# Kernel optimization log

Hardware: AMD Instinct MI355X
Metric: run time of the kernel (lower is better)

## Reference

```python
import jax, jax.numpy as jnp
import numpy as np

B, N, IN_DIM, SLOT_DIM, NUM_SLOTS, NUM_ITERS = 64, 4096, 256, 256, 8, 3
LN_EPS = 1e-5


def _ln(x, g, b):
    m = jnp.mean(x, axis=-1, keepdims=True)
    v = jnp.mean(jnp.square(x - m), axis=-1, keepdims=True)
    return (x - m) * jax.lax.rsqrt(v + LN_EPS) * g + b


def setup_inputs() -> dict:
    key = jax.random.key(0)
    ks = jax.random.split(key, 16)
    D, I = SLOT_DIM, IN_DIM
    s = 0.02
    return {
        "inputs": jax.random.normal(ks[0], (B, N, I), jnp.float32),
        "slots_noise": jax.random.normal(ks[1], (B, NUM_SLOTS, D), jnp.float32),
        "slots_mu": jax.random.normal(ks[2], (1, 1, D), jnp.float32),
        "slots_log_sigma": jnp.zeros((1, 1, D), jnp.float32),
        "ln_in_g": jnp.ones((I,), jnp.float32), "ln_in_b": jnp.zeros((I,), jnp.float32),
        "ln_s_g": jnp.ones((D,), jnp.float32), "ln_s_b": jnp.zeros((D,), jnp.float32),
        "ln_m_g": jnp.ones((D,), jnp.float32), "ln_m_b": jnp.zeros((D,), jnp.float32),
        "Wq": jax.random.normal(ks[3], (D, D), jnp.float32) * s,
        "Wk": jax.random.normal(ks[4], (I, D), jnp.float32) * s,
        "Wv": jax.random.normal(ks[5], (I, D), jnp.float32) * s,
        "gru_w_ih": jax.random.normal(ks[6], (3 * D, D), jnp.float32) * s,
        "gru_w_hh": jax.random.normal(ks[7], (3 * D, D), jnp.float32) * s,
        "gru_b_ih": jnp.zeros((3 * D,), jnp.float32),
        "gru_b_hh": jnp.zeros((3 * D,), jnp.float32),
        "mlp_w1": jax.random.normal(ks[8], (D, 4 * D), jnp.float32) * s,
        "mlp_b1": jnp.zeros((4 * D,), jnp.float32),
        "mlp_w2": jax.random.normal(ks[9], (4 * D, D), jnp.float32) * s,
        "mlp_b2": jnp.zeros((D,), jnp.float32),
    }


def reference(inputs, slots_noise, slots_mu, slots_log_sigma, ln_in_g, ln_in_b,
              ln_s_g, ln_s_b, ln_m_g, ln_m_b, Wq, Wk, Wv,
              gru_w_ih, gru_w_hh, gru_b_ih, gru_b_hh,
              mlp_w1, mlp_b1, mlp_w2, mlp_b2):
    D = SLOT_DIM
    # slot init: mu + sigma * noise
    slots = slots_mu + jnp.exp(slots_log_sigma) * slots_noise  # [B, S, D]
    x = _ln(inputs, ln_in_g, ln_in_b)                          # [B, N, I]
    k = x @ Wk                                                 # [B, N, D]
    v = x @ Wv                                                 # [B, N, D]
    scale = 1.0 / jnp.sqrt(jnp.float32(D))
    attn = None
    for _ in range(NUM_ITERS):
        slots_prev = slots
        s_n = _ln(slots, ln_s_g, ln_s_b)
        q = s_n @ Wq                                           # [B, S, D]
        logits = jnp.einsum('bnd,bmd->bnm', k, q) * scale      # [B, N, S]
        attn = jax.nn.softmax(logits, axis=-1)                 # softmax over slots
        attn_nrm = attn / (jnp.sum(attn, axis=1, keepdims=True) + 1e-8)
        updates = jnp.einsum('bnm,bnd->bmd', attn_nrm, v)      # [B, S, D]
        # GRUCell (PyTorch semantics)
        gi = updates @ gru_w_ih.T + gru_b_ih                   # [B, S, 3D]
        gh = slots_prev @ gru_w_hh.T + gru_b_hh
        gi_r, gi_z, gi_n = jnp.split(gi, 3, axis=-1)
        gh_r, gh_z, gh_n = jnp.split(gh, 3, axis=-1)
        r = jax.nn.sigmoid(gi_r + gh_r)
        z = jax.nn.sigmoid(gi_z + gh_z)
        n = jnp.tanh(gi_n + r * gh_n)
        slots = (1.0 - z) * n + z * slots_prev
        # residual MLP
        h = jax.nn.relu(_ln(slots, ln_m_g, ln_m_b) @ mlp_w1 + mlp_b1)
        slots = slots + h @ mlp_w2 + mlp_b2
    return slots, jnp.transpose(attn, (0, 2, 1))
```

## Files before the change

### kernel.cpp

```cpp
#include <hip/hip_runtime.h>


typedef unsigned short u16;
typedef __attribute__((ext_vector_type(8))) short bf16x8;
typedef __attribute__((ext_vector_type(4))) float f32x4;

#define MFMA16(a, b, c) __builtin_amdgcn_mfma_f32_16x16x32_bf16((a), (b), (c), 0, 0, 0)

__device__ __forceinline__ u16 f2bf(float f) {
  union { float f; unsigned u; } v; v.f = f;
  unsigned r = (v.u + 0x7fffu + ((v.u >> 16) & 1u)) >> 16;
  return (u16)r;
}
__device__ __forceinline__ float sigm(float x) { return 1.f / (1.f + __expf(-x)); }
__device__ __forceinline__ float tanh_f(float x) { return 1.f - 2.f / (1.f + __expf(2.f * x)); }

__global__ __launch_bounds__(256) void prep_kernel(
    const float* __restrict__ Wq, const float* __restrict__ Wk, const float* __restrict__ Wv,
    const float* __restrict__ wih, const float* __restrict__ whh,
    const float* __restrict__ w1, const float* __restrict__ w2,
    u16* __restrict__ wkB, u16* __restrict__ wqT, u16* __restrict__ wvT,
    u16* __restrict__ wihB, u16* __restrict__ whhB, u16* __restrict__ w1T, u16* __restrict__ w2T) {
  const int bid = blockIdx.x;
  const int tid = threadIdx.x;
  if (bid < 160) {
    __shared__ float tile[64][65];
    const float* src; u16* dst; int R, C, t;
    if (bid < 16)      { src = Wq; dst = wqT; R = 256;  C = 256;  t = bid; }
    else if (bid < 32) { src = Wv; dst = wvT; R = 256;  C = 256;  t = bid - 16; }
    else if (bid < 96) { src = w1; dst = w1T; R = 1024; C = 256;  t = bid - 32; }
    else               { src = w2; dst = w2T; R = 256;  C = 1024; t = bid - 96; }
    const int tilesJ = C >> 6;
    const int i0 = (t / tilesJ) * 64, j0 = (t % tilesJ) * 64;
    const int c = tid & 63, r0 = tid >> 6;
#pragma unroll
    for (int rr = 0; rr < 16; rr++) {
      int row = rr * 4 + r0;
      tile[row][c] = src[(size_t)(j0 + row) * R + i0 + c];
    }
    __syncthreads();
#pragma unroll
    for (int rr = 0; rr < 16; rr++) {
      int row = rr * 4 + r0;
      dst[(size_t)(i0 + row) * C + j0 + c] = f2bf(tile[c][row]);
    }
  } else {
    int gid = (bid - 160) * 256 + tid;
    for (int i4 = gid; i4 < 114688; i4 += 64 * 256) {
      int i = i4 * 4;
      const float* s; u16* d; int off;
      if (i < 65536) { s = Wk; d = wkB; off = i; }
      else if (i < 262144) { s = wih; d = wihB; off = i - 65536; }
      else { s = whh; d = whhB; off = i - 262144; }
      float4 v = *reinterpret_cast<const float4*>(s + off);
      unsigned lo = (unsigned)f2bf(v.x) | ((unsigned)f2bf(v.y) << 16);
      unsigned hi = (unsigned)f2bf(v.z) | ((unsigned)f2bf(v.w) << 16);
      *reinterpret_cast<uint2*>(d + off) = make_uint2(lo, hi);
    }
  }
}

__device__ __forceinline__ void ln_row16(const float (*src)[264], u16 (*dst)[264],
                                         const float* __restrict__ g, const float* __restrict__ bb,
                                         int wave, int lane) {
  int row = wave;
  if (row < 8) {
    float4 v = *reinterpret_cast<const float4*>(&src[row][lane * 4]);
    float s = v.x + v.y + v.z + v.w;
    float sq = v.x * v.x + v.y * v.y + v.z * v.z + v.w * v.w;
#pragma unroll
    for (int m = 1; m < 64; m <<= 1) { s += __shfl_xor(s, m); sq += __shfl_xor(sq, m); }
    float mu = s * (1.f / 256.f);
    float var = sq * (1.f / 256.f) - mu * mu;
    float rstd = rsqrtf(fmaxf(var, 0.f) + 1e-5f);
    float4 gg = *reinterpret_cast<const float4*>(&g[lane * 4]);
    float4 bv = *reinterpret_cast<const float4*>(&bb[lane * 4]);
    unsigned lo = (unsigned)f2bf((v.x - mu) * rstd * gg.x + bv.x) |
                  ((unsigned)f2bf((v.y - mu) * rstd * gg.y + bv.y) << 16);
    unsigned hi = (unsigned)f2bf((v.z - mu) * rstd * gg.z + bv.z) |
                  ((unsigned)f2bf((v.w - mu) * rstd * gg.w + bv.w) << 16);
    *reinterpret_cast<uint2*>(&dst[row][lane * 4]) = make_uint2(lo, hi);
  } else if (row < 16) {
    *reinterpret_cast<uint2*>(&dst[row][lane * 4]) = make_uint2(0, 0);
  }
}

__global__ __launch_bounds__(1024, 4) void slot_kernel(
    float* __restrict__ slots, u16* __restrict__ qg, float* __restrict__ cd,
    const float* __restrict__ wsY, const float* __restrict__ wsS,
    const u16* __restrict__ wvT, const u16* __restrict__ wihB, const u16* __restrict__ whhB,
    const u16* __restrict__ w1T, const u16* __restrict__ w2T, const u16* __restrict__ wqT,
    const u16* __restrict__ wkB,
    const float* __restrict__ bih, const float* __restrict__ bhh,
    const float* __restrict__ b1v, const float* __restrict__ b2v,
    const float* __restrict__ g_in, const float* __restrict__ b_in,
    const float* __restrict__ g_s, const float* __restrict__ b_s,
    const float* __restrict__ g_m, const float* __restrict__ b_m,
    const float* __restrict__ s_mu, const float* __restrict__ s_ls,
    const float* __restrict__ noise,
    float* __restrict__ d_out, int do_update) {
  __shared__ alignas(16) char pool[58368];
  u16 (*h_lds)[1032] = reinterpret_cast<u16(*)[1032]>(pool);
  u16 (*u_lds)[264] = reinterpret_cast<u16(*)[264]>(pool);
  u16 (*uv_lds)[264] = reinterpret_cast<u16(*)[264]>(pool + 8448);
  u16 (*sb_lds)[264] = reinterpret_cast<u16(*)[264]>(pool + 16896);
  u16 (*m_lds)[264] = reinterpret_cast<u16(*)[264]>(pool + 33024);
  float (*ns_lds)[264] = reinterpret_cast<float(*)[264]>(pool + 41472);
  u16 (*q_lds)[264] = reinterpret_cast<u16(*)[264]>(pool + 41472);
  __shared__ float sS0[16], sS1[16], sInv[16];
  __shared__ float redq[16][4][4][2];

  const int b = blockIdx.x;
  const int tid = threadIdx.x;
  const int lane = tid & 63, wave = tid >> 6;
  const int quad = lane >> 4, col = lane & 15;
  const int i256 = tid & 255, s4 = tid >> 8;
  const f32x4 vzero = {0.f, 0.f, 0.f, 0.f};

  if (do_update) {
    if (tid < 16) {
      float S0 = 0.f, S1 = 0.f;
      if (tid < 8) {
        for (int c = 0; c < 8; c++) {
          S0 += wsS[((b * 8 + c) * 8 + tid) * 2 + 0];
          S1 += wsS[((b * 8 + c) * 8 + tid) * 2 + 1];
        }
      }
      sS0[tid] = S0; sS1[tid] = S1; sInv[tid] = 1.f / (S0 + 1e-8f);
    }
#pragma unroll
    for (int r = 0; r < 4; r++) {
      int s = s4 + r * 4;
      sb_lds[s][i256] = (s < 8) ? f2bf(slots[(size_t)(b * 8 + s) * 256 + i256]) : (u16)0;
    }
    __syncthreads();
    {
      float gv = g_in[i256], bv = b_in[i256];
#pragma unroll
      for (int r = 0; r < 4; r++) {
        int s = s4 + r * 4;
        if (s < 8) {
          float y = 0.f;
#pragma unroll
          for (int c = 0; c < 8; c++) y += wsY[((size_t)((b * 8 + c) * 8 + s)) * 256 + i256];
          u_lds[s][i256] = f2bf((gv * (y - sS1[s]) + bv * sS0[s]) * sInv[s]);
        } else {
          u_lds[s][i256] = 0;
        }
      }
    }
    __syncthreads();
    {
      bf16x8 af[8];
#pragma unroll
      for (int k = 0; k < 8; k++)
        af[k] = *reinterpret_cast<const bf16x8*>(&u_lds[col][k * 32 + quad * 8]);
      int ct = wave;
      f32x4 acc = vzero;
#pragma unroll
      for (int k = 0; k < 8; k++) {
        bf16x8 bf = *reinterpret_cast<const bf16x8*>(wvT + (size_t)(ct * 16 + col) * 256 + k * 32 + quad * 8);
        acc = MFMA16(af[k], bf, acc);
      }
#pragma unroll
      for (int r = 0; r < 4; r++) {
        int s = quad * 4 + r;
        uv_lds[s][ct * 16 + col] = (s < 8) ? f2bf(acc[r]) : (u16)0;
      }
    }
    __syncthreads();
    {
      bf16x8 afu[8], afs[8];
#pragma unroll
      for (int k = 0; k < 8; k++) {
        afu[k] = *reinterpret_cast<const bf16x8*>(&uv_lds[col][k * 32 + quad * 8]);
        afs[k] = *reinterpret_cast<const bf16x8*>(&sb_lds[col][k * 32 + quad * 8]);
      }
      int d = wave * 16 + col;
      f32x4 a_ir = vzero, a_iz = vzero, a_in = vzero, a_hr = vzero, a_hz = vzero, a_hn = vzero;
#pragma unroll
      for (int k = 0; k < 8; k++) {
        int ko = k * 32 + quad * 8;
        a_ir = MFMA16(afu[k], *reinterpret_cast<const bf16x8*>(wihB + (size_t)(d)*256 + ko), a_ir);
        a_iz = MFMA16(afu[k], *reinterpret_cast<const bf16x8*>(wihB + (size_t)(256 + d) * 256 + ko), a_iz);
        a_in = MFMA16(afu[k], *reinterpret_cast<const bf16x8*>(wihB + (size_t)(512 + d) * 256 + ko), a_in);
        a_hr = MFMA16(afs[k], *reinterpret_cast<const bf16x8*>(whhB + (size_t)(d)*256 + ko), a_hr);
        a_hz = MFMA16(afs[k], *reinterpret_cast<const bf16x8*>(whhB + (size_t)(256 + d) * 256 + ko), a_hz);
        a_hn = MFMA16(afs[k], *reinterpret_cast<const bf16x8*>(whhB + (size_t)(512 + d) * 256 + ko), a_hn);
      }
      float bihr = bih[d], bihz = bih[256 + d], bihn = bih[512 + d];
      float bhhr = bhh[d], bhhz = bhh[256 + d], bhhn = bhh[512 + d];
#pragma unroll
      for (int r = 0; r < 4; r++) {
        int s = quad * 4 + r;
        float rg = sigm(a_ir[r] + bihr + a_hr[r] + bhhr);
        float zg = sigm(a_iz[r] + bihz + a_hz[r] + bhhz);
        float ng = tanh_f(a_in[r] + bihn + rg * (a_hn[r] + bhhn));
        float prev = (s < 8) ? slots[(size_t)(b * 8 + s) * 256 + d] : 0.f;
        float ns = (1.f - zg) * ng + zg * prev;
        ns_lds[s][d] = (s < 8) ? ns : 0.f;
      }
    }
    __syncthreads();
    ln_row16(ns_lds, m_lds, g_m, b_m, wave, lane);
    __syncthreads();
    {
      bf16x8 af[8];
#pragma unroll
      for (int k = 0; k < 8; k++)
        af[k] = *reinterpret_cast<const bf16x8*>(&m_lds[col][k * 32 + quad * 8]);
      for (int cc = 0; cc < 4; cc++) {
        int ct = wave * 4 + cc;
        f32x4 acc = vzero;
#pragma unroll
        for (int k = 0; k < 8; k++) {
          bf16x8 bf = *reinterpret_cast<const bf16x8*>(w1T + (size_t)(ct * 16 + col) * 256 + k * 32 + quad * 8);
          acc = MFMA16(af[k], bf, acc);
        }
        float bb = b1v[ct * 16 + col];
#pragma unroll
        for (int r = 0; r < 4; r++) {
          int s = quad * 4 + r;
          float h = fmaxf(acc[r] + bb, 0.f);
          h_lds[s][ct * 16 + col] = (s < 8) ? f2bf(h) : (u16)0;
        }
      }
    }
    __syncthreads();
    {
      int ct = wave;
      f32x4 acc = vzero;
      for (int k = 0; k < 32; k++) {
        bf16x8 af = *reinterpret_cast<const bf16x8*>(&h_lds[col][k * 32 + quad * 8]);
        bf16x8 bf = *reinterpret_cast<const bf16x8*>(w2T + (size_t)(ct * 16 + col) * 1024 + k * 32 + quad * 8);
        acc = MFMA16(af, bf, acc);
      }
      int d = ct * 16 + col;
      float bb = b2v[d];
#pragma unroll
      for (int r = 0; r < 4; r++) {
        int s = quad * 4 + r;
        if (s < 8) {
          float fin = ns_lds[s][d] + acc[r] + bb;
          slots[(size_t)(b * 8 + s) * 256 + d] = fin;
          d_out[(size_t)(b * 8 + s) * 256 + d] = fin;
          ns_lds[s][d] = fin;
        }
      }
    }
    __syncthreads();
  } else {
#pragma unroll
    for (int r = 0; r < 4; r++) {
      int s = s4 + r * 4;
      float v = 0.f;
      if (s < 8) {
        v = s_mu[i256] + __expf(s_ls[i256]) * noise[(size_t)(b * 8 + s) * 256 + i256];
        slots[(size_t)(b * 8 + s) * 256 + i256] = v;
      }
      ns_lds[s][i256] = v;
    }
    __syncthreads();
  }

  ln_row16(ns_lds, m_lds, g_s, b_s, wave, lane);
  __syncthreads();
  {
    bf16x8 af[8];
#pragma unroll
    for (int k = 0; k < 8; k++)
      af[k] = *reinterpret_cast<const bf16x8*>(&m_lds[col][k * 32 + quad * 8]);
    int ct = wave;
    f32x4 acc = vzero;
#pragma unroll
    for (int k = 0; k < 8; k++) {
      bf16x8 bf = *reinterpret_cast<const bf16x8*>(wqT + (size_t)(ct * 16 + col) * 256 + k * 32 + quad * 8);
      acc = MFMA16(af[k], bf, acc);
    }
#pragma unroll
    for (int r = 0; r < 4; r++) {
      int s = quad * 4 + r;
      q_lds[s][ct * 16 + col] = (s < 8) ? f2bf(acc[r]) : (u16)0;
    }
  }
  __syncthreads();
  {
    bf16x8 af[8];
#pragma unroll
    for (int k = 0; k < 8; k++)
      af[k] = *reinterpret_cast<const bf16x8*>(&q_lds[col][k * 32 + quad * 8]);
    float cacc[4] = {0.f, 0.f, 0.f, 0.f}, dacc[4] = {0.f, 0.f, 0.f, 0.f};
    int ct = wave;
    f32x4 acc = vzero;
#pragma unroll
    for (int k = 0; k < 8; k++) {
      bf16x8 bf = *reinterpret_cast<const bf16x8*>(wkB + (size_t)(ct * 16 + col) * 256 + k * 32 + quad * 8);
      acc = MFMA16(af[k], bf, acc);
    }
    int i = ct * 16 + col;
    float gi_ = g_in[i] * 0.0625f, bi_ = b_in[i] * 0.0625f;
#pragma unroll
    for (int r = 0; r < 4; r++) {
      int s = quad * 4 + r;
      float qkv = acc[r];
      float qgv = (s < 8) ? gi_ * qkv : 0.f;
      qg[(size_t)(b * 16 + s) * 256 + i] = f2bf(qgv);
      cacc[r] -= qgv;
      dacc[r] += (s < 8) ? bi_ * qkv : 0.f;
    }
#pragma unroll
    for (int r = 0; r < 4; r++) {
#pragma unroll
      for (int m = 1; m < 16; m <<= 1) {
        cacc[r] += __shfl_xor(cacc[r], m);
        dacc[r] += __shfl_xor(dacc[r], m);
      }
    }
    if (col == 0) {
#pragma unroll
      for (int r = 0; r < 4; r++) {
        redq[wave][quad][r][0] = cacc[r];
        redq[wave][quad][r][1] = dacc[r];
      }
    }
    __syncthreads();
    if (tid < 16) {
      int qd = tid >> 2, r = tid & 3;
      float c = 0.f, dd = 0.f;
      for (int w = 0; w < 16; w++) { c += redq[w][qd][r][0]; dd += redq[w][qd][r][1]; }
      cd[(b * 16 + tid) * 2 + 0] = c;
      cd[(b * 16 + tid) * 2 + 1] = dd;
    }
  }
}

template <int PASS>
__global__ __launch_bounds__(512, 4) void attn_kernel(
    const float* __restrict__ x, u16* __restrict__ xb, float2* __restrict__ stats2,
    const u16* __restrict__ qg, const float* __restrict__ cd,
    float* __restrict__ out, float* __restrict__ wsY, float* __restrict__ wsS) {
  __shared__ alignas(16) u16 x_lds[64][264];
  __shared__ alignas(16) u16 a2t[16][72];
  __shared__ float2 stats_lds[64];
  __shared__ float2 red2[4][8];

  const int chunk = blockIdx.x, b = blockIdx.y;
  const int tid = threadIdx.x;
  const int lane = tid & 63, wave = tid >> 6;
  const int quad = lane >> 4, col = lane & 15;

  for (int idx = tid; idx < 288; idx += 512)
    reinterpret_cast<unsigned*>(&a2t[8][0])[idx] = 0;

  bf16x8 bfrag[8];
#pragma unroll
  for (int k = 0; k < 8; k++)
    bfrag[k] = *reinterpret_cast<const bf16x8*>(qg + (size_t)(b * 16 + col) * 256 + k * 32 + quad * 8);
  const float2 cdv = *reinterpret_cast<const float2*>(cd + (b * 16 + col) * 2);

  f32x4 Yacc[2];
  Yacc[0] = {0.f, 0.f, 0.f, 0.f};
  Yacc[1] = {0.f, 0.f, 0.f, 0.f};
  float s0a = 0.f, s1a = 0.f;
  float* out_attn = out + 131072;

  float4 pf0[8];
  uint2 pf1[8];
  float2 pfs;
  {
    const int nb0 = chunk * 512;
    if (PASS == 0) {
#pragma unroll
      for (int p = 0; p < 8; p++)
        pf0[p] = *reinterpret_cast<const float4*>(x + (size_t)(b * 4096 + nb0 + wave * 8 + p) * 256 + lane * 4);
    } else {
#pragma unroll
      for (int p = 0; p < 8; p++)
        pf1[p] = *reinterpret_cast<const uint2*>(xb + (size_t)(b * 4096 + nb0 + wave * 8 + p) * 256 + lane * 4);
      if (tid < 64) pfs = stats2[(size_t)b * 4096 + nb0 + tid];
    }
  }

  for (int g = 0; g < 8; g++) {
    const int nb = chunk * 512 + g * 64;
    __syncthreads();
    if (PASS == 0) {
#pragma unroll
      for (int p = 0; p < 8; p++) {
        int row = wave * 8 + p;
        float4 v = pf0[p];
        float s = v.x + v.y + v.z + v.w;
        float sq = v.x * v.x + v.y * v.y + v.z * v.z + v.w * v.w;
#pragma unroll
        for (int m = 1; m < 64; m <<= 1) { s += __shfl_xor(s, m); sq += __shfl_xor(sq, m); }
        float mu = s * (1.f / 256.f);
        float var = sq * (1.f / 256.f) - mu * mu;
        float rstd = rsqrtf(fmaxf(var, 0.f) + 1e-5f);
        float2 st = make_float2(rstd, rstd * mu);
        if (lane == 0) {
          stats_lds[row] = st;
          stats2[(size_t)b * 4096 + nb + row] = st;
        }
        unsigned lo = (unsigned)f2bf(v.x) | ((unsigned)f2bf(v.y) << 16);
        unsigned hi = (unsigned)f2bf(v.z) | ((unsigned)f2bf(v.w) << 16);
        *reinterpret_cast<uint2*>(&x_lds[row][lane * 4]) = make_uint2(lo, hi);
        *reinterpret_cast<uint2*>(xb + (size_t)(b * 4096 + nb + row) * 256 + lane * 4) = make_uint2(lo, hi);
      }
    } else {
#pragma unroll
      for (int p = 0; p < 8; p++) {
        int row = wave * 8 + p;
        *reinterpret_cast<uint2*>(&x_lds[row][lane * 4]) = pf1[p];
      }
      if (tid < 64) stats_lds[tid] = pfs;
    }
    __syncthreads();
    if (g < 7) {
      const int nbn = nb + 64;
      if (PASS == 0) {
#pragma unroll
        for (int p = 0; p < 8; p++)
          pf0[p] = *reinterpret_cast<const float4*>(x + (size_t)(b * 4096 + nbn + wave * 8 + p) * 256 + lane * 4);
      } else {
#pragma unroll
        for (int p = 0; p < 8; p++)
          pf1[p] = *reinterpret_cast<const uint2*>(xb + (size_t)(b * 4096 + nbn + wave * 8 + p) * 256 + lane * 4);
        if (tid < 64) pfs = stats2[(size_t)b * 4096 + nbn + tid];
      }
    }
    if (wave < 4) {
      const int rowbase = wave * 16;
      f32x4 acc = {0.f, 0.f, 0.f, 0.f};
#pragma unroll
      for (int k = 0; k < 8; k++) {
        bf16x8 af = *reinterpret_cast<const bf16x8*>(&x_lds[rowbase + col][k * 32 + quad * 8]);
        acc = MFMA16(af, bfrag[k], acc);
      }
      float at[4], rmx[4], rmy[4];
#pragma unroll
      for (int r = 0; r < 4; r++) {
        float2 rm = stats_lds[rowbase + quad * 4 + r];
        rmx[r] = rm.x; rmy[r] = rm.y;
        float lg = rm.x * acc[r] + rm.y * cdv.x + cdv.y;
        float mx = lg;
        mx = fmaxf(mx, __shfl_xor(mx, 1));
        mx = fmaxf(mx, __shfl_xor(mx, 2));
        mx = fmaxf(mx, __shfl_xor(mx, 4));
        float e = __expf(lg - mx);
        float sm = e;
        sm += __shfl_xor(sm, 1); sm += __shfl_xor(sm, 2); sm += __shfl_xor(sm, 4);
        at[r] = e / sm;
      }
      if (col < 8) {
#pragma unroll
        for (int r = 0; r < 4; r++) {
          int n_loc = rowbase + quad * 4 + r;
          out_attn[(size_t)(b * 8 + col) * 4096 + nb + n_loc] = at[r];
          a2t[col][n_loc] = f2bf(at[r] * rmx[r]);
          s0a += at[r];
          s1a += at[r] * rmy[r];
        }
      }
    }
    __syncthreads();
    {
      bf16x8 af0 = *reinterpret_cast<const bf16x8*>(&a2t[col][quad * 8]);
      bf16x8 af1 = *reinterpret_cast<const bf16x8*>(&a2t[col][32 + quad * 8]);
#pragma unroll
      for (int cc = 0; cc < 2; cc++) {
        int ib = (wave * 2 + cc) * 16 + col;
        union { short s[8]; bf16x8 v; } b0, b1;
#pragma unroll
        for (int j = 0; j < 8; j++) {
          b0.s[j] = (short)x_lds[quad * 8 + j][ib];
          b1.s[j] = (short)x_lds[32 + quad * 8 + j][ib];
        }
        Yacc[cc] = MFMA16(af0, b0.v, Yacc[cc]);
        Yacc[cc] = MFMA16(af1, b1.v, Yacc[cc]);
      }
    }
  }
  if (quad < 2) {
#pragma unroll
    for (int cc = 0; cc < 2; cc++) {
      int i = (wave * 2 + cc) * 16 + col;
#pragma unroll
      for (int r = 0; r < 4; r++) {
        int s = quad * 4 + r;
        wsY[(size_t)((b * 8 + chunk) * 8 + s) * 256 + i] = Yacc[cc][r];
      }
    }
  }
  s0a += __shfl_xor(s0a, 16); s0a += __shfl_xor(s0a, 32);
  s1a += __shfl_xor(s1a, 16); s1a += __shfl_xor(s1a, 32);
  if (wave < 4 && lane < 8) red2[wave][lane] = make_float2(s0a, s1a);
  __syncthreads();
  if (tid < 8) {
    float S0 = 0.f, S1 = 0.f;
#pragma unroll
    for (int w = 0; w < 4; w++) { S0 += red2[w][tid].x; S1 += red2[w][tid].y; }
    wsS[((b * 8 + chunk) * 8 + tid) * 2 + 0] = S0;
    wsS[((b * 8 + chunk) * 8 + tid) * 2 + 1] = S1;
  }
}

extern "C" void kernel_launch(void* const* d_in, const int* in_sizes, int n_in,
                              void* d_out, int out_size, void* d_ws, size_t ws_size,
                              hipStream_t stream) {
  const float* inputs = (const float*)d_in[0];
  const float* noise = (const float*)d_in[1];
  const float* s_mu = (const float*)d_in[2];
  const float* s_ls = (const float*)d_in[3];
  const float* g_in = (const float*)d_in[4];
  const float* b_in = (const float*)d_in[5];
  const float* g_s = (const float*)d_in[6];
  const float* b_s = (const float*)d_in[7];
  const float* g_m = (const float*)d_in[8];
  const float* b_m = (const float*)d_in[9];
  const float* Wq = (const float*)d_in[10];
  const float* Wk = (const float*)d_in[11];
  const float* Wv = (const float*)d_in[12];
  const float* wih = (const float*)d_in[13];
  const float* whh = (const float*)d_in[14];
  const float* bih = (const float*)d_in[15];
  const float* bhh = (const float*)d_in[16];
  const float* w1 = (const float*)d_in[17];
  const float* b1v = (const float*)d_in[18];
  const float* w2 = (const float*)d_in[19];
  const float* b2v = (const float*)d_in[20];
  float* out = (float*)d_out;

  size_t o = 0;
  auto take = [&](size_t bytes) {
    void* p = (char*)d_ws + o;
    o += (bytes + 255) & ~(size_t)255;
    return p;
  };
  float* slots = (float*)take((size_t)64 * 8 * 256 * 4);
  u16* qg = (u16*)take((size_t)64 * 16 * 256 * 2);
  float* cd = (float*)take((size_t)64 * 16 * 2 * 4);
  float* wsY = (float*)take((size_t)64 * 8 * 8 * 256 * 4);
  float* wsS = (float*)take((size_t)64 * 8 * 8 * 2 * 4);
  u16* wkB = (u16*)take((size_t)65536 * 2);
  u16* wqT = (u16*)take((size_t)65536 * 2);
  u16* wvT = (u16*)take((size_t)65536 * 2);
  u16* wihB = (u16*)take((size_t)196608 * 2);
  u16* whhB = (u16*)take((size_t)196608 * 2);
  u16* w1T = (u16*)take((size_t)262144 * 2);
  u16* w2T = (u16*)take((size_t)262144 * 2);
  u16* xb = (u16*)take((size_t)64 * 4096 * 256 * 2);
  float2* stats2 = (float2*)take((size_t)64 * 4096 * 8);

  prep_kernel<<<224, 256, 0, stream>>>(Wq, Wk, Wv, wih, whh, w1, w2,
                                       wkB, wqT, wvT, wihB, whhB, w1T, w2T);
  slot_kernel<<<64, 1024, 0, stream>>>(slots, qg, cd, wsY, wsS,
                                       wvT, wihB, whhB, w1T, w2T, wqT, wkB,
                                       bih, bhh, b1v, b2v,
                                       g_in, b_in, g_s, b_s, g_m, b_m,
                                       s_mu, s_ls, noise, out, 0);
  for (int it = 0; it < 3; it++) {
    if (it == 0)
      attn_kernel<0><<<dim3(8, 64), 512, 0, stream>>>(inputs, xb, stats2, qg, cd, out, wsY, wsS);
    else
      attn_kernel<1><<<dim3(8, 64), 512, 0, stream>>>(inputs, xb, stats2, qg, cd, out, wsY, wsS);
    slot_kernel<<<64, 1024, 0, stream>>>(slots, qg, cd, wsY, wsS,
                                         wvT, wihB, whhB, w1T, w2T, wqT, wkB,
                                         bih, bhh, b1v, b2v,
                                         g_in, b_in, g_s, b_s, g_m, b_m,
                                         s_mu, s_ls, noise, out, 1);
  }
}
```

Baseline: 701.9 us.

## Double attention grid chunks, halve slot block, compute LN stats via MFMA

```diff
diff --git a/kernel.cpp b/kernel.cpp
--- a/kernel.cpp
+++ b/kernel.cpp
@@ -60,32 +60,29 @@
   }
 }
 
-__device__ __forceinline__ void ln_row16(const float (*src)[264], u16 (*dst)[264],
+__device__ __forceinline__ void ln_row8w(const float (*src)[264], u16 (*dst)[264],
                                          const float* __restrict__ g, const float* __restrict__ bb,
                                          int wave, int lane) {
   int row = wave;
-  if (row < 8) {
-    float4 v = *reinterpret_cast<const float4*>(&src[row][lane * 4]);
-    float s = v.x + v.y + v.z + v.w;
-    float sq = v.x * v.x + v.y * v.y + v.z * v.z + v.w * v.w;
-#pragma unroll
-    for (int m = 1; m < 64; m <<= 1) { s += __shfl_xor(s, m); sq += __shfl_xor(sq, m); }
-    float mu = s * (1.f / 256.f);
-    float var = sq * (1.f / 256.f) - mu * mu;
-    float rstd = rsqrtf(fmaxf(var, 0.f) + 1e-5f);
-    float4 gg = *reinterpret_cast<const float4*>(&g[lane * 4]);
-    float4 bv = *reinterpret_cast<const float4*>(&bb[lane * 4]);
-    unsigned lo = (unsigned)f2bf((v.x - mu) * rstd * gg.x + bv.x) |
-                  ((unsigned)f2bf((v.y - mu) * rstd * gg.y + bv.y) << 16);
-    unsigned hi = (unsigned)f2bf((v.z - mu) * rstd * gg.z + bv.z) |
-                  ((unsigned)f2bf((v.w - mu) * rstd * gg.w + bv.w) << 16);
-    *reinterpret_cast<uint2*>(&dst[row][lane * 4]) = make_uint2(lo, hi);
-  } else if (row < 16) {
-    *reinterpret_cast<uint2*>(&dst[row][lane * 4]) = make_uint2(0, 0);
-  }
+  float4 v = *reinterpret_cast<const float4*>(&src[row][lane * 4]);
+  float s = v.x + v.y + v.z + v.w;
+  float sq = v.x * v.x + v.y * v.y + v.z * v.z + v.w * v.w;
+#pragma unroll
+  for (int m = 1; m < 64; m <<= 1) { s += __shfl_xor(s, m); sq += __shfl_xor(sq, m); }
+  float mu = s * (1.f / 256.f);
+  float var = sq * (1.f / 256.f) - mu * mu;
+  float rstd = rsqrtf(fmaxf(var, 0.f) + 1e-5f);
+  float4 gg = *reinterpret_cast<const float4*>(&g[lane * 4]);
+  float4 bv = *reinterpret_cast<const float4*>(&bb[lane * 4]);
+  unsigned lo = (unsigned)f2bf((v.x - mu) * rstd * gg.x + bv.x) |
+                ((unsigned)f2bf((v.y - mu) * rstd * gg.y + bv.y) << 16);
+  unsigned hi = (unsigned)f2bf((v.z - mu) * rstd * gg.z + bv.z) |
+                ((unsigned)f2bf((v.w - mu) * rstd * gg.w + bv.w) << 16);
+  *reinterpret_cast<uint2*>(&dst[row][lane * 4]) = make_uint2(lo, hi);
+  *reinterpret_cast<uint2*>(&dst[row + 8][lane * 4]) = make_uint2(0, 0);
 }
 
-__global__ __launch_bounds__(1024, 4) void slot_kernel(
+__global__ __launch_bounds__(512, 2) void slot_kernel(
     float* __restrict__ slots, u16* __restrict__ qg, float* __restrict__ cd,
     const float* __restrict__ wsY, const float* __restrict__ wsS,
     const u16* __restrict__ wvT, const u16* __restrict__ wihB, const u16* __restrict__ whhB,
@@ -108,7 +105,7 @@
   float (*ns_lds)[264] = reinterpret_cast<float(*)[264]>(pool + 41472);
   u16 (*q_lds)[264] = reinterpret_cast<u16(*)[264]>(pool + 41472);
   __shared__ float sS0[16], sS1[16], sInv[16];
-  __shared__ float redq[16][4][4][2];
+  __shared__ float redq[8][4][4][2];
 
   const int b = blockIdx.x;
   const int tid = threadIdx.x;
@@ -121,28 +118,28 @@
     if (tid < 16) {
       float S0 = 0.f, S1 = 0.f;
       if (tid < 8) {
-        for (int c = 0; c < 8; c++) {
-          S0 += wsS[((b * 8 + c) * 8 + tid) * 2 + 0];
-          S1 += wsS[((b * 8 + c) * 8 + tid) * 2 + 1];
+        for (int c = 0; c < 16; c++) {
+          S0 += wsS[((b * 16 + c) * 8 + tid) * 2 + 0];
+          S1 += wsS[((b * 16 + c) * 8 + tid) * 2 + 1];
         }
       }
       sS0[tid] = S0; sS1[tid] = S1; sInv[tid] = 1.f / (S0 + 1e-8f);
     }
 #pragma unroll
-    for (int r = 0; r < 4; r++) {
-      int s = s4 + r * 4;
+    for (int r = 0; r < 8; r++) {
+      int s = r * 2 + s4;
       sb_lds[s][i256] = (s < 8) ? f2bf(slots[(size_t)(b * 8 + s) * 256 + i256]) : (u16)0;
     }
     __syncthreads();
     {
       float gv = g_in[i256], bv = b_in[i256];
 #pragma unroll
-      for (int r = 0; r < 4; r++) {
-        int s = s4 + r * 4;
+      for (int r = 0; r < 8; r++) {
+        int s = r * 2 + s4;
         if (s < 8) {
           float y = 0.f;
 #pragma unroll
-          for (int c = 0; c < 8; c++) y += wsY[((size_t)((b * 8 + c) * 8 + s)) * 256 + i256];
+          for (int c = 0; c < 16; c++) y += wsY[((size_t)((b * 16 + c) * 8 + s)) * 256 + i256];
           u_lds[s][i256] = f2bf((gv * (y - sS1[s]) + bv * sS0[s]) * sInv[s]);
         } else {
           u_lds[s][i256] = 0;
@@ -155,17 +152,20 @@
 #pragma unroll
       for (int k = 0; k < 8; k++)
         af[k] = *reinterpret_cast<const bf16x8*>(&u_lds[col][k * 32 + quad * 8]);
-      int ct = wave;
-      f32x4 acc = vzero;
-#pragma unroll
-      for (int k = 0; k < 8; k++) {
-        bf16x8 bf = *reinterpret_cast<const bf16x8*>(wvT + (size_t)(ct * 16 + col) * 256 + k * 32 + quad * 8);
-        acc = MFMA16(af[k], bf, acc);
-      }
-#pragma unroll
-      for (int r = 0; r < 4; r++) {
-        int s = quad * 4 + r;
-        uv_lds[s][ct * 16 + col] = (s < 8) ? f2bf(acc[r]) : (u16)0;
+#pragma unroll
+      for (int cc = 0; cc < 2; cc++) {
+        int ct = wave * 2 + cc;
+        f32x4 acc = vzero;
+#pragma unroll
+        for (int k = 0; k < 8; k++) {
+          bf16x8 bf = *reinterpret_cast<const bf16x8*>(wvT + (size_t)(ct * 16 + col) * 256 + k * 32 + quad * 8);
+          acc = MFMA16(af[k], bf, acc);
+        }
+#pragma unroll
+        for (int r = 0; r < 4; r++) {
+          int s = quad * 4 + r;
+          uv_lds[s][ct * 16 + col] = (s < 8) ? f2bf(acc[r]) : (u16)0;
+        }
       }
     }
     __syncthreads();
@@ -176,41 +176,43 @@
         afu[k] = *reinterpret_cast<const bf16x8*>(&uv_lds[col][k * 32 + quad * 8]);
         afs[k] = *reinterpret_cast<const bf16x8*>(&sb_lds[col][k * 32 + quad * 8]);
       }
-      int d = wave * 16 + col;
-      f32x4 a_ir = vzero, a_iz = vzero, a_in = vzero, a_hr = vzero, a_hz = vzero, a_hn = vzero;
-#pragma unroll
-      for (int k = 0; k < 8; k++) {
-        int ko = k * 32 + quad * 8;
-        a_ir = MFMA16(afu[k], *reinterpret_cast<const bf16x8*>(wihB + (size_t)(d)*256 + ko), a_ir);
-        a_iz = MFMA16(afu[k], *reinterpret_cast<const bf16x8*>(wihB + (size_t)(256 + d) * 256 + ko), a_iz);
-        a_in = MFMA16(afu[k], *reinterpret_cast<const bf16x8*>(wihB + (size_t)(512 + d) * 256 + ko), a_in);
-        a_hr = MFMA16(afs[k], *reinterpret_cast<const bf16x8*>(whhB + (size_t)(d)*256 + ko), a_hr);
-        a_hz = MFMA16(afs[k], *reinterpret_cast<const bf16x8*>(whhB + (size_t)(256 + d) * 256 + ko), a_hz);
-        a_hn = MFMA16(afs[k], *reinterpret_cast<const bf16x8*>(whhB + (size_t)(512 + d) * 256 + ko), a_hn);
-      }
-      float bihr = bih[d], bihz = bih[256 + d], bihn = bih[512 + d];
-      float bhhr = bhh[d], bhhz = bhh[256 + d], bhhn = bhh[512 + d];
-#pragma unroll
-      for (int r = 0; r < 4; r++) {
-        int s = quad * 4 + r;
-        float rg = sigm(a_ir[r] + bihr + a_hr[r] + bhhr);
-        float zg = sigm(a_iz[r] + bihz + a_hz[r] + bhhz);
-        float ng = tanh_f(a_in[r] + bihn + rg * (a_hn[r] + bhhn));
-        float prev = (s < 8) ? slots[(size_t)(b * 8 + s) * 256 + d] : 0.f;
-        float ns = (1.f - zg) * ng + zg * prev;
-        ns_lds[s][d] = (s < 8) ? ns : 0.f;
-      }
-    }
-    __syncthreads();
-    ln_row16(ns_lds, m_lds, g_m, b_m, wave, lane);
+      for (int cc = 0; cc < 2; cc++) {
+        int d = (wave * 2 + cc) * 16 + col;
+        f32x4 a_ir = vzero, a_iz = vzero, a_in = vzero, a_hr = vzero, a_hz = vzero, a_hn = vzero;
+#pragma unroll
+        for (int k = 0; k < 8; k++) {
+          int ko = k * 32 + quad * 8;
+          a_ir = MFMA16(afu[k], *reinterpret_cast<const bf16x8*>(wihB + (size_t)(d)*256 + ko), a_ir);
+          a_iz = MFMA16(afu[k], *reinterpret_cast<const bf16x8*>(wihB + (size_t)(256 + d) * 256 + ko), a_iz);
+          a_in = MFMA16(afu[k], *reinterpret_cast<const bf16x8*>(wihB + (size_t)(512 + d) * 256 + ko), a_in);
+          a_hr = MFMA16(afs[k], *reinterpret_cast<const bf16x8*>(whhB + (size_t)(d)*256 + ko), a_hr);
+          a_hz = MFMA16(afs[k], *reinterpret_cast<const bf16x8*>(whhB + (size_t)(256 + d) * 256 + ko), a_hz);
+          a_hn = MFMA16(afs[k], *reinterpret_cast<const bf16x8*>(whhB + (size_t)(512 + d) * 256 + ko), a_hn);
+        }
+        float bihr = bih[d], bihz = bih[256 + d], bihn = bih[512 + d];
+        float bhhr = bhh[d], bhhz = bhh[256 + d], bhhn = bhh[512 + d];
+#pragma unroll
+        for (int r = 0; r < 4; r++) {
+          int s = quad * 4 + r;
+          float rg = sigm(a_ir[r] + bihr + a_hr[r] + bhhr);
+          float zg = sigm(a_iz[r] + bihz + a_hz[r] + bhhz);
+          float ng = tanh_f(a_in[r] + bihn + rg * (a_hn[r] + bhhn));
+          float prev = (s < 8) ? slots[(size_t)(b * 8 + s) * 256 + d] : 0.f;
+          float ns = (1.f - zg) * ng + zg * prev;
+          ns_lds[s][d] = (s < 8) ? ns : 0.f;
+        }
+      }
+    }
+    __syncthreads();
+    ln_row8w(ns_lds, m_lds, g_m, b_m, wave, lane);
     __syncthreads();
     {
       bf16x8 af[8];
 #pragma unroll
       for (int k = 0; k < 8; k++)
         af[k] = *reinterpret_cast<const bf16x8*>(&m_lds[col][k * 32 + quad * 8]);
-      for (int cc = 0; cc < 4; cc++) {
-        int ct = wave * 4 + cc;
+      for (int cc = 0; cc < 8; cc++) {
+        int ct = wave * 8 + cc;
         f32x4 acc = vzero;
 #pragma unroll
         for (int k = 0; k < 8; k++) {
@@ -227,8 +229,8 @@
       }
     }
     __syncthreads();
-    {
-      int ct = wave;
+    for (int cc = 0; cc < 2; cc++) {
+      int ct = wave * 2 + cc;
       f32x4 acc = vzero;
       for (int k = 0; k < 32; k++) {
         bf16x8 af = *reinterpret_cast<const bf16x8*>(&h_lds[col][k * 32 + quad * 8]);
@@ -251,8 +253,8 @@
     __syncthreads();
   } else {
 #pragma unroll
-    for (int r = 0; r < 4; r++) {
-      int s = s4 + r * 4;
+    for (int r = 0; r < 8; r++) {
+      int s = r * 2 + s4;
       float v = 0.f;
       if (s < 8) {
         v = s_mu[i256] + __expf(s_ls[i256]) * noise[(size_t)(b * 8 + s) * 256 + i256];
@@ -263,24 +265,27 @@
     __syncthreads();
   }
 
-  ln_row16(ns_lds, m_lds, g_s, b_s, wave, lane);
+  ln_row8w(ns_lds, m_lds, g_s, b_s, wave, lane);
   __syncthreads();
   {
     bf16x8 af[8];
 #pragma unroll
     for (int k = 0; k < 8; k++)
       af[k] = *reinterpret_cast<const bf16x8*>(&m_lds[col][k * 32 + quad * 8]);
-    int ct = wave;
-    f32x4 acc = vzero;
-#pragma unroll
-    for (int k = 0; k < 8; k++) {
-      bf16x8 bf = *reinterpret_cast<const bf16x8*>(wqT + (size_t)(ct * 16 + col) * 256 + k * 32 + quad * 8);
-      acc = MFMA16(af[k], bf, acc);
-    }
-#pragma unroll
-    for (int r = 0; r < 4; r++) {
-      int s = quad * 4 + r;
-      q_lds[s][ct * 16 + col] = (s < 8) ? f2bf(acc[r]) : (u16)0;
+#pragma unroll
+    for (int cc = 0; cc < 2; cc++) {
+      int ct = wave * 2 + cc;
+      f32x4 acc = vzero;
+#pragma unroll
+      for (int k = 0; k < 8; k++) {
+        bf16x8 bf = *reinterpret_cast<const bf16x8*>(wqT + (size_t)(ct * 16 + col) * 256 + k * 32 + quad * 8);
+        acc = MFMA16(af[k], bf, acc);
+      }
+#pragma unroll
+      for (int r = 0; r < 4; r++) {
+        int s = quad * 4 + r;
+        q_lds[s][ct * 16 + col] = (s < 8) ? f2bf(acc[r]) : (u16)0;
+      }
     }
   }
   __syncthreads();
@@ -290,23 +295,26 @@
     for (int k = 0; k < 8; k++)
       af[k] = *reinterpret_cast<const bf16x8*>(&q_lds[col][k * 32 + quad * 8]);
     float cacc[4] = {0.f, 0.f, 0.f, 0.f}, dacc[4] = {0.f, 0.f, 0.f, 0.f};
-    int ct = wave;
-    f32x4 acc = vzero;
-#pragma unroll
-    for (int k = 0; k < 8; k++) {
-      bf16x8 bf = *reinterpret_cast<const bf16x8*>(wkB + (size_t)(ct * 16 + col) * 256 + k * 32 + quad * 8);
-      acc = MFMA16(af[k], bf, acc);
-    }
-    int i = ct * 16 + col;
-    float gi_ = g_in[i] * 0.0625f, bi_ = b_in[i] * 0.0625f;
-#pragma unroll
-    for (int r = 0; r < 4; r++) {
-      int s = quad * 4 + r;
-      float qkv = acc[r];
-      float qgv = (s < 8) ? gi_ * qkv : 0.f;
-      qg[(size_t)(b * 16 + s) * 256 + i] = f2bf(qgv);
-      cacc[r] -= qgv;
-      dacc[r] += (s < 8) ? bi_ * qkv : 0.f;
+#pragma unroll
+    for (int cc = 0; cc < 2; cc++) {
+      int ct = wave * 2 + cc;
+      f32x4 acc = vzero;
+#pragma unroll
+      for (int k = 0; k < 8; k++) {
+        bf16x8 bf = *reinterpret_cast<const bf16x8*>(wkB + (size_t)(ct * 16 + col) * 256 + k * 32 + quad * 8);
+        acc = MFMA16(af[k], bf, acc);
+      }
+      int i = ct * 16 + col;
+      float gi_ = g_in[i] * 0.0625f, bi_ = b_in[i] * 0.0625f;
+#pragma unroll
+      for (int r = 0; r < 4; r++) {
+        int s = quad * 4 + r;
+        float qkv = acc[r];
+        float qgv = (s < 8) ? gi_ * qkv : 0.f;
+        qg[(size_t)(b * 16 + s) * 256 + i] = f2bf(qgv);
+        cacc[r] -= qgv;
+        dacc[r] += (s < 8) ? bi_ * qkv : 0.f;
+      }
     }
 #pragma unroll
     for (int r = 0; r < 4; r++) {
@@ -327,7 +335,7 @@
     if (tid < 16) {
       int qd = tid >> 2, r = tid & 3;
       float c = 0.f, dd = 0.f;
-      for (int w = 0; w < 16; w++) { c += redq[w][qd][r][0]; dd += redq[w][qd][r][1]; }
+      for (int w = 0; w < 8; w++) { c += redq[w][qd][r][0]; dd += redq[w][qd][r][1]; }
       cd[(b * 16 + tid) * 2 + 0] = c;
       cd[(b * 16 + tid) * 2 + 1] = dd;
     }
@@ -335,7 +343,7 @@
 }
 
 template <int PASS>
-__global__ __launch_bounds__(512, 4) void attn_kernel(
+__global__ __launch_bounds__(512, PASS == 0 ? 4 : 6) void attn_kernel(
     const float* __restrict__ x, u16* __restrict__ xb, float2* __restrict__ stats2,
     const u16* __restrict__ qg, const float* __restrict__ cd,
     float* __restrict__ out, float* __restrict__ wsY, float* __restrict__ wsS) {
@@ -352,10 +360,6 @@
   for (int idx = tid; idx < 288; idx += 512)
     reinterpret_cast<unsigned*>(&a2t[8][0])[idx] = 0;
 
-  bf16x8 bfrag[8];
-#pragma unroll
-  for (int k = 0; k < 8; k++)
-    bfrag[k] = *reinterpret_cast<const bf16x8*>(qg + (size_t)(b * 16 + col) * 256 + k * 32 + quad * 8);
   const float2 cdv = *reinterpret_cast<const float2*>(cd + (b * 16 + col) * 2);
 
   f32x4 Yacc[2];
@@ -368,7 +372,7 @@
   uint2 pf1[8];
   float2 pfs;
   {
-    const int nb0 = chunk * 512;
+    const int nb0 = chunk * 256;
     if (PASS == 0) {
 #pragma unroll
       for (int p = 0; p < 8; p++)
@@ -381,26 +385,14 @@
     }
   }
 
-  for (int g = 0; g < 8; g++) {
-    const int nb = chunk * 512 + g * 64;
+  for (int g = 0; g < 4; g++) {
+    const int nb = chunk * 256 + g * 64;
     __syncthreads();
     if (PASS == 0) {
 #pragma unroll
       for (int p = 0; p < 8; p++) {
         int row = wave * 8 + p;
         float4 v = pf0[p];
-        float s = v.x + v.y + v.z + v.w;
-        float sq = v.x * v.x + v.y * v.y + v.z * v.z + v.w * v.w;
-#pragma unroll
-        for (int m = 1; m < 64; m <<= 1) { s += __shfl_xor(s, m); sq += __shfl_xor(sq, m); }
-        float mu = s * (1.f / 256.f);
-        float var = sq * (1.f / 256.f) - mu * mu;
-        float rstd = rsqrtf(fmaxf(var, 0.f) + 1e-5f);
-        float2 st = make_float2(rstd, rstd * mu);
-        if (lane == 0) {
-          stats_lds[row] = st;
-          stats2[(size_t)b * 4096 + nb + row] = st;
-        }
         unsigned lo = (unsigned)f2bf(v.x) | ((unsigned)f2bf(v.y) << 16);
         unsigned hi = (unsigned)f2bf(v.z) | ((unsigned)f2bf(v.w) << 16);
         *reinterpret_cast<uint2*>(&x_lds[row][lane * 4]) = make_uint2(lo, hi);
@@ -415,7 +407,7 @@
       if (tid < 64) stats_lds[tid] = pfs;
     }
     __syncthreads();
-    if (g < 7) {
+    if (g < 3) {
       const int nbn = nb + 64;
       if (PASS == 0) {
 #pragma unroll
@@ -430,18 +422,50 @@
     }
     if (wave < 4) {
       const int rowbase = wave * 16;
+      bf16x8 af[8], bfrag[8];
+#pragma unroll
+      for (int k = 0; k < 8; k++) {
+        af[k] = *reinterpret_cast<const bf16x8*>(&x_lds[rowbase + col][k * 32 + quad * 8]);
+        bfrag[k] = *reinterpret_cast<const bf16x8*>(qg + (size_t)(b * 16 + col) * 256 + k * 32 + quad * 8);
+      }
       f32x4 acc = {0.f, 0.f, 0.f, 0.f};
 #pragma unroll
-      for (int k = 0; k < 8; k++) {
-        bf16x8 af = *reinterpret_cast<const bf16x8*>(&x_lds[rowbase + col][k * 32 + quad * 8]);
-        acc = MFMA16(af, bfrag[k], acc);
-      }
-      float at[4], rmx[4], rmy[4];
+      for (int k = 0; k < 8; k++) acc = MFMA16(af[k], bfrag[k], acc);
+
+      float rmx[4], rmy[4];
+      if (PASS == 0) {
+        const short one_bf = (short)0x3F80;
+        bf16x8 ones8 = {one_bf, one_bf, one_bf, one_bf, one_bf, one_bf, one_bf, one_bf};
+        f32x4 accS = {0.f, 0.f, 0.f, 0.f}, accG = {0.f, 0.f, 0.f, 0.f};
+#pragma unroll
+        for (int k = 0; k < 8; k++) {
+          accS = MFMA16(af[k], ones8, accS);
+          accG = MFMA16(af[k], af[k], accG);
+        }
+#pragma unroll
+        for (int r = 0; r < 4; r++) {
+          float sq = __shfl(accG[r], (quad << 4) + quad * 4 + r);
+          float mu = accS[r] * (1.f / 256.f);
+          float var = sq * (1.f / 256.f) - mu * mu;
+          float rstd = rsqrtf(fmaxf(var, 0.f) + 1e-5f);
+          rmx[r] = rstd; rmy[r] = rstd * mu;
+        }
+        if (col == 0) {
+#pragma unroll
+          for (int r = 0; r < 4; r++)
+            stats2[(size_t)b * 4096 + nb + rowbase + quad * 4 + r] = make_float2(rmx[r], rmy[r]);
+        }
+      } else {
+#pragma unroll
+        for (int r = 0; r < 4; r++) {
+          float2 rm = stats_lds[rowbase + quad * 4 + r];
+          rmx[r] = rm.x; rmy[r] = rm.y;
+        }
+      }
+      float at[4];
 #pragma unroll
       for (int r = 0; r < 4; r++) {
-        float2 rm = stats_lds[rowbase + quad * 4 + r];
-        rmx[r] = rm.x; rmy[r] = rm.y;
-        float lg = rm.x * acc[r] + rm.y * cdv.x + cdv.y;
+        float lg = rmx[r] * acc[r] + rmy[r] * cdv.x + cdv.y;
         float mx = lg;
         mx = fmaxf(mx, __shfl_xor(mx, 1));
         mx = fmaxf(mx, __shfl_xor(mx, 2));
@@ -487,7 +511,7 @@
 #pragma unroll
       for (int r = 0; r < 4; r++) {
         int s = quad * 4 + r;
-        wsY[(size_t)((b * 8 + chunk) * 8 + s) * 256 + i] = Yacc[cc][r];
+        wsY[(size_t)((b * 16 + chunk) * 8 + s) * 256 + i] = Yacc[cc][r];
       }
     }
   }
@@ -499,8 +523,8 @@
     float S0 = 0.f, S1 = 0.f;
 #pragma unroll
     for (int w = 0; w < 4; w++) { S0 += red2[w][tid].x; S1 += red2[w][tid].y; }
-    wsS[((b * 8 + chunk) * 8 + tid) * 2 + 0] = S0;
-    wsS[((b * 8 + chunk) * 8 + tid) * 2 + 1] = S1;
+    wsS[((b * 16 + chunk) * 8 + tid) * 2 + 0] = S0;
+    wsS[((b * 16 + chunk) * 8 + tid) * 2 + 1] = S1;
   }
 }
 
@@ -539,8 +563,8 @@
   float* slots = (float*)take((size_t)64 * 8 * 256 * 4);
   u16* qg = (u16*)take((size_t)64 * 16 * 256 * 2);
   float* cd = (float*)take((size_t)64 * 16 * 2 * 4);
-  float* wsY = (float*)take((size_t)64 * 8 * 8 * 256 * 4);
-  float* wsS = (float*)take((size_t)64 * 8 * 8 * 2 * 4);
+  float* wsY = (float*)take((size_t)64 * 16 * 8 * 256 * 4);
+  float* wsS = (float*)take((size_t)64 * 16 * 8 * 2 * 4);
   u16* wkB = (u16*)take((size_t)65536 * 2);
   u16* wqT = (u16*)take((size_t)65536 * 2);
   u16* wvT = (u16*)take((size_t)65536 * 2);
@@ -553,20 +577,20 @@
 
   prep_kernel<<<224, 256, 0, stream>>>(Wq, Wk, Wv, wih, whh, w1, w2,
                                        wkB, wqT, wvT, wihB, whhB, w1T, w2T);
-  slot_kernel<<<64, 1024, 0, stream>>>(slots, qg, cd, wsY, wsS,
-                                       wvT, wihB, whhB, w1T, w2T, wqT, wkB,
-                                       bih, bhh, b1v, b2v,
-                                       g_in, b_in, g_s, b_s, g_m, b_m,
-                                       s_mu, s_ls, noise, out, 0);
+  slot_kernel<<<64, 512, 0, stream>>>(slots, qg, cd, wsY, wsS,
+                                      wvT, wihB, whhB, w1T, w2T, wqT, wkB,
+                                      bih, bhh, b1v, b2v,
+                                      g_in, b_in, g_s, b_s, g_m, b_m,
+                                      s_mu, s_ls, noise, out, 0);
   for (int it = 0; it < 3; it++) {
     if (it == 0)
-      attn_kernel<0><<<dim3(8, 64), 512, 0, stream>>>(inputs, xb, stats2, qg, cd, out, wsY, wsS);
+      attn_kernel<0><<<dim3(16, 64), 512, 0, stream>>>(inputs, xb, stats2, qg, cd, out, wsY, wsS);
     else
-      attn_kernel<1><<<dim3(8, 64), 512, 0, stream>>>(inputs, xb, stats2, qg, cd, out, wsY, wsS);
-    slot_kernel<<<64, 1024, 0, stream>>>(slots, qg, cd, wsY, wsS,
-                                         wvT, wihB, whhB, w1T, w2T, wqT, wkB,
-                                         bih, bhh, b1v, b2v,
-                                         g_in, b_in, g_s, b_s, g_m, b_m,
-                                         s_mu, s_ls, noise, out, 1);
+      attn_kernel<1><<<dim3(16, 64), 512, 0, stream>>>(inputs, xb, stats2, qg, cd, out, wsY, wsS);
+    slot_kernel<<<64, 512, 0, stream>>>(slots, qg, cd, wsY, wsS,
+                                        wvT, wihB, whhB, w1T, w2T, wqT, wkB,
+                                        bih, bhh, b1v, b2v,
+                                        g_in, b_in, g_s, b_s, g_m, b_m,
+                                        s_mu, s_ls, noise, out, 1);
   }
 }
```

Result: slower. 803.7 us (+14.5%).
